# Optimization experiments

Measured on AMD Instinct MI355X. Metric: run time of the kernel, lower is better.

The kernel has to match this reference:

```python
import jax, jax.numpy as jnp
import numpy as np

H = 2880      # hidden_size
NH = 64       # num query heads
NKV = 8       # num kv heads
D = 64        # head_dim
G = NH // NKV # GQA group size
W = 128       # sliding window (keys per query, incl. self)
THETA = 150000.0
N = 1024      # tokens


def setup_inputs() -> dict:
    key = jax.random.key(0)
    k0, k1, k2, k3 = jax.random.split(key, 4)
    hidden_states = jax.random.normal(k0, (N, H), jnp.float32)
    Wqkv = jax.random.normal(k1, (H, (NH + 2 * NKV) * D), jnp.float32) * (H ** -0.5)
    Wo = jax.random.normal(k2, (NH * D, H), jnp.float32) * ((NH * D) ** -0.5)
    sinks = jax.random.normal(k3, (NH,), jnp.float32)
    positions = jnp.arange(N, dtype=jnp.int64)
    return {"hidden_states": hidden_states, "Wqkv": Wqkv, "Wo": Wo,
            "sinks": sinks, "positions": positions}


def _rope(x, pos):
    # NeoX-style rotary over full head_dim. x: [n, h, D], pos: [n]
    half = D // 2
    inv_freq = 1.0 / (THETA ** (jnp.arange(half, dtype=jnp.float32) / half))
    ang = pos[:, None].astype(jnp.float32) * inv_freq          # [n, half]
    cos = jnp.cos(ang)[:, None, :]
    sin = jnp.sin(ang)[:, None, :]
    x1, x2 = x[..., :half], x[..., half:]
    return jnp.concatenate([x1 * cos - x2 * sin, x2 * cos + x1 * sin], axis=-1)


def reference(hidden_states, Wqkv, Wo, sinks, positions):
    n = hidden_states.shape[0]
    qkv = hidden_states @ Wqkv
    q, k, v = jnp.split(qkv, [NH * D, NH * D + NKV * D], axis=-1)
    q = _rope(q.reshape(n, NH, D), positions)   # [n, NH, D]
    k = _rope(k.reshape(n, NKV, D), positions)  # [n, NKV, D]
    v = v.reshape(n, NKV, D)

    # Sliding-window key indices: query i attends keys j in [i-W+1, i]
    idx = positions[:, None] - (W - 1) + jnp.arange(W)[None, :]  # [n, W]
    valid = idx >= 0
    idx = jnp.clip(idx, 0, n - 1)
    k_win = k[idx]  # [n, W, NKV, D]
    v_win = v[idx]  # [n, W, NKV, D]

    qg = q.reshape(n, NKV, G, D)
    scores = jnp.einsum('nkgd,nwkd->nkgw', qg, k_win) * (D ** -0.5)
    scores = jnp.where(valid[:, None, None, :], scores, -jnp.inf)

    # Attention sinks: softmax over [scores, sink_logit]; sink gets no value.
    sink = sinks.reshape(NKV, G)                      # [NKV, G]
    m = jnp.maximum(scores.max(-1), sink[None])       # [n, NKV, G]
    p = jnp.exp(scores - m[..., None])                # [n, NKV, G, W]
    denom = p.sum(-1) + jnp.exp(sink[None] - m)       # [n, NKV, G]
    out = jnp.einsum('nkgw,nwkd->nkgd', p, v_win) / denom[..., None]
    return out.reshape(n, NH * D) @ Wo
```

## Files before the change

kernel.cpp:

```cpp
#include <hip/hip_runtime.h>
#include <hip/hip_bf16.h>

#define HDIM   2880
#define NH     64
#define NKV    8
#define DHEAD  64
#define GQ     (NH / NKV)
#define WIN    128
#define NTOK   1024
#define QKV_N  ((NH + 2 * NKV) * DHEAD)
#define QCOLS  (NH * DHEAD)
#define KOFF   QCOLS
#define VOFF   (QCOLS + NKV * DHEAD)

typedef __attribute__((ext_vector_type(8))) short short8;
typedef __attribute__((ext_vector_type(4))) float floatx4;

__device__ unsigned short g_Xb   [(size_t)NTOK  * HDIM];
__device__ unsigned short g_qkvb [(size_t)NTOK  * QKV_N];
__device__ unsigned short g_attn [(size_t)NTOK  * QCOLS];
__device__ unsigned short g_WqkvT[(size_t)QKV_N * HDIM];
__device__ unsigned short g_WoT  [(size_t)HDIM * QCOLS];

__device__ __forceinline__ unsigned short f2b(float f) {
    __hip_bfloat16 h = __float2bfloat16(f);
    return *reinterpret_cast<unsigned short*>(&h);
}

__device__ __forceinline__ void gload_lds16(const unsigned short* g, unsigned short* l) {
    __builtin_amdgcn_global_load_lds(
        (const __attribute__((address_space(1))) unsigned int*)g,
        (__attribute__((address_space(3))) unsigned int*)l, 16, 0, 0);
}

__global__ __launch_bounds__(256) void transpose_cvt(
        const float* __restrict__ in, unsigned short* __restrict__ out,
        int K, int N) {
    int bk = blockIdx.x, bn = blockIdx.y;
    int t = threadIdx.x;
    __shared__ __align__(16) unsigned short T[64 * 72];
    #pragma unroll
    for (int i = 0; i < 4; ++i) {
        int c = i * 256 + t;
        int r = c >> 4, cc = (c & 15) * 4;
        float4 v = *(const float4*)(in + (size_t)(bk * 64 + r) * N + bn * 64 + cc);
        T[r * 72 + cc + 0] = f2b(v.x);
        T[r * 72 + cc + 1] = f2b(v.y);
        T[r * 72 + cc + 2] = f2b(v.z);
        T[r * 72 + cc + 3] = f2b(v.w);
    }
    __syncthreads();
    #pragma unroll
    for (int i = 0; i < 2; ++i) {
        int c = i * 256 + t;
        int rn = c >> 3, kc = (c & 7) * 8;
        int4 vv;
        unsigned short* tp = (unsigned short*)&vv;
        #pragma unroll
        for (int j = 0; j < 8; ++j) tp[j] = T[(kc + j) * 72 + rn];
        *(int4*)(out + (size_t)(bn * 64 + rn) * K + bk * 64 + kc) = vv;
    }
}

__global__ __launch_bounds__(256) void cvt_bf16(
        const float* __restrict__ in, unsigned short* __restrict__ out, int n4) {
    int id = blockIdx.x * 256 + threadIdx.x;
    if (id >= n4) return;
    float4 v = *(const float4*)(in + (size_t)id * 4);
    ushort4 o;
    o.x = f2b(v.x); o.y = f2b(v.y); o.z = f2b(v.z); o.w = f2b(v.w);
    *(ushort4*)(out + (size_t)id * 4) = o;
}

template<int KLEN, int MODE, int NBN>
__global__ __launch_bounds__(256) void gemm_dir(
        const unsigned short* __restrict__ A, const unsigned short* __restrict__ Bt,
        void* __restrict__ outp) {
    int d0 = blockIdx.x;
    int work = (d0 & 7) * NBN + (d0 >> 3);
    int bm = work & 7, bn = work >> 3;
    int t = threadIdx.x, lane = t & 63, wid = t >> 6;
    int quad = lane >> 4, ml = lane & 15;
    __shared__ __align__(16) unsigned short As[128 * 64];
    __shared__ __align__(16) unsigned short Bs[64 * 64];
    floatx4 acc[2][4];
    #pragma unroll
    for (int i = 0; i < 2; ++i)
        #pragma unroll
        for (int j = 0; j < 4; ++j) acc[i][j] = (floatx4){0.f, 0.f, 0.f, 0.f};

    int srow = lane >> 3;
    int scol = (lane & 7) * 8;
    const unsigned short* Ab = A  + (size_t)(bm * 128) * KLEN;
    const unsigned short* Bb = Bt + (size_t)(bn * 64) * KLEN;

    for (int k0 = 0; k0 < KLEN; k0 += 64) {
        #pragma unroll
        for (int j = 0; j < 4; ++j) {
            int grp = wid * 4 + j;
            int r = grp * 8 + srow;
            gload_lds16(Ab + (size_t)r * KLEN + k0 + scol, &As[grp * 512]);
        }
        #pragma unroll
        for (int j = 0; j < 2; ++j) {
            int grp = wid * 2 + j;
            int r = grp * 8 + srow;
            gload_lds16(Bb + (size_t)r * KLEN + k0 + scol, &Bs[grp * 512]);
        }
        __syncthreads();
        #pragma unroll
        for (int kk = 0; kk < 64; kk += 32) {
            short8 af[2], bf[4];
            #pragma unroll
            for (int mt = 0; mt < 2; ++mt)
                af[mt] = *(const short8*)&As[(wid * 32 + mt * 16 + ml) * 64 + kk + quad * 8];
            #pragma unroll
            for (int nt = 0; nt < 4; ++nt)
                bf[nt] = *(const short8*)&Bs[(nt * 16 + ml) * 64 + kk + quad * 8];
            #pragma unroll
            for (int mt = 0; mt < 2; ++mt)
                #pragma unroll
                for (int nt = 0; nt < 4; ++nt)
                    acc[mt][nt] = __builtin_amdgcn_mfma_f32_16x16x32_bf16(af[mt], bf[nt], acc[mt][nt], 0, 0, 0);
        }
        __syncthreads();
    }

    if constexpr (MODE == 0) {
        unsigned short* qp = (unsigned short*)outp;
        int cb = bn * 64;
        if (bn < NH + NKV) {
            float inv0 = expf(-(float)ml * 0.3724497053f);
            float inv1 = expf(-(float)(16 + ml) * 0.3724497053f);
            #pragma unroll
            for (int mt = 0; mt < 2; ++mt) {
                #pragma unroll
                for (int r = 0; r < 4; ++r) {
                    int n = bm * 128 + wid * 32 + mt * 16 + quad * 4 + r;
                    unsigned short* op = qp + (size_t)n * QKV_N + cb;
                    float s0, c0, s1, c1;
                    sincosf((float)n * inv0, &s0, &c0);
                    sincosf((float)n * inv1, &s1, &c1);
                    float x1a = acc[mt][0][r], x2a = acc[mt][2][r];
                    float x1b = acc[mt][1][r], x2b = acc[mt][3][r];
                    op[ml]           = f2b(x1a * c0 - x2a * s0);
                    op[ml + 32]      = f2b(x2a * c0 + x1a * s0);
                    op[16 + ml]      = f2b(x1b * c1 - x2b * s1);
                    op[16 + ml + 32] = f2b(x2b * c1 + x1b * s1);
                }
            }
        } else {
            #pragma unroll
            for (int mt = 0; mt < 2; ++mt)
                #pragma unroll
                for (int r = 0; r < 4; ++r) {
                    int n = bm * 128 + wid * 32 + mt * 16 + quad * 4 + r;
                    unsigned short* op = qp + (size_t)n * QKV_N + cb;
                    #pragma unroll
                    for (int nt = 0; nt < 4; ++nt)
                        op[nt * 16 + ml] = f2b(acc[mt][nt][r]);
                }
        }
    } else {
        float* op0 = (float*)outp;
        #pragma unroll
        for (int mt = 0; mt < 2; ++mt)
            #pragma unroll
            for (int r = 0; r < 4; ++r) {
                int n = bm * 128 + wid * 32 + mt * 16 + quad * 4 + r;
                float* op = op0 + (size_t)n * HDIM + bn * 64;
                #pragma unroll
                for (int nt = 0; nt < 4; ++nt)
                    op[nt * 16 + ml] = acc[mt][nt][r];
            }
    }
}

#define TQ     16
#define WROWS  160
#define KS_LD  72
#define VT_LD  168
#define PS_LD  168

__global__ __launch_bounds__(256) void attn_mfma(
        const unsigned short* __restrict__ qkvb,
        const float* __restrict__ sinks,
        unsigned short* __restrict__ aout) {
    int d0 = blockIdx.x;
    int work = (d0 & 7) * 64 + (d0 >> 3);
    int t0 = (work & 63) * TQ, kh = work >> 6;
    int t = threadIdx.x, lane = t & 63, wid = t >> 6;
    int quad = lane >> 4, ml = lane & 15;
    int wavebase = wid * 32;

    __shared__ __align__(16) unsigned short Ks[WROWS * KS_LD];
    __shared__ __align__(16) unsigned short Vt[DHEAD * VT_LD];
    __shared__ __align__(16) unsigned short Ps[4 * 16 * PS_LD];
    unsigned short* Psw = &Ps[wid * 16 * PS_LD];

    #pragma unroll
    for (int i = 0; i < 5; ++i) {
        int c = i * 256 + t;
        int w = c >> 3, d8 = (c & 7) * 8;
        int r = t0 - 127 + w;
        r = min(max(r, 0), NTOK - 1);
        *(int4*)&Ks[w * KS_LD + d8] =
            *(const int4*)(qkvb + (size_t)r * QKV_N + KOFF + kh * DHEAD + d8);
        int4 vv = *(const int4*)(qkvb + (size_t)r * QKV_N + VOFF + kh * DHEAD + d8);
        const unsigned short* vp = (const unsigned short*)&vv;
        #pragma unroll
        for (int j = 0; j < 8; ++j) Vt[(d8 + j) * VT_LD + w] = vp[j];
    }
    __syncthreads();

    short8 qf[2][2];
    #pragma unroll
    for (int mt = 0; mt < 2; ++mt) {
        int m = wavebase + mt * 16 + ml;
        int tl = m & 15, g = m >> 4;
        const unsigned short* qp = qkvb + (size_t)(t0 + tl) * QKV_N + (kh * GQ + g) * DHEAD;
        #pragma unroll
        for (int kk = 0; kk < 2; ++kk)
            qf[mt][kk] = *(const short8*)(qp + kk * 32 + quad * 8);
    }

    floatx4 S[2][10];
    #pragma unroll
    for (int mt = 0; mt < 2; ++mt)
        #pragma unroll
        for (int nt = 0; nt < 10; ++nt) S[mt][nt] = (floatx4){0.f, 0.f, 0.f, 0.f};
    #pragma unroll
    for (int kk = 0; kk < 2; ++kk) {
        #pragma unroll
        for (int nt = 0; nt < 10; ++nt) {
            short8 kb = *(const short8*)&Ks[(nt * 16 + ml) * KS_LD + kk * 32 + quad * 8];
            #pragma unroll
            for (int mt = 0; mt < 2; ++mt)
                S[mt][nt] = __builtin_amdgcn_mfma_f32_16x16x32_bf16(qf[mt][kk], kb, S[mt][nt], 0, 0, 0);
        }
    }

    int wmin0 = 127 - t0;
    #pragma unroll
    for (int mt = 0; mt < 2; ++mt) {
        #pragma unroll
        for (int r = 0; r < 4; ++r) {
            int tl = (wavebase + mt * 16 + quad * 4 + r) & 15;
            int wlo = tl > wmin0 ? tl : wmin0;
            int whi = tl + 127;
            #pragma unroll
            for (int nt = 0; nt < 10; ++nt) {
                int w = nt * 16 + ml;
                float s = S[mt][nt][r] * 0.125f;
                S[mt][nt][r] = (w >= wlo && w <= whi) ? s : -INFINITY;
            }
        }
    }

    #pragma unroll
    for (int mt = 0; mt < 2; ++mt) {
        int g = (wavebase + mt * 16) >> 4;
        float sk = sinks[kh * GQ + g];
        #pragma unroll
        for (int r = 0; r < 4; ++r) {
            float rm = -INFINITY;
            #pragma unroll
            for (int nt = 0; nt < 10; ++nt) rm = fmaxf(rm, S[mt][nt][r]);
            #pragma unroll
            for (int off = 1; off < 16; off <<= 1) rm = fmaxf(rm, __shfl_xor(rm, off));
            rm = fmaxf(rm, sk);
            float sum = 0.f;
            #pragma unroll
            for (int nt = 0; nt < 10; ++nt) {
                float p = __expf(S[mt][nt][r] - rm);
                S[mt][nt][r] = p;
                sum += p;
            }
            #pragma unroll
            for (int off = 1; off < 16; off <<= 1) sum += __shfl_xor(sum, off);
            float inv = 1.f / (sum + __expf(sk - rm));
            #pragma unroll
            for (int nt = 0; nt < 10; ++nt) S[mt][nt][r] *= inv;
        }
    }

    #pragma unroll
    for (int mt = 0; mt < 2; ++mt) {
        #pragma unroll
        for (int r = 0; r < 4; ++r) {
            int lr = quad * 4 + r;
            #pragma unroll
            for (int nt = 0; nt < 10; ++nt)
                Psw[lr * PS_LD + nt * 16 + ml] = f2b(S[mt][nt][r]);
        }
        floatx4 O[4];
        #pragma unroll
        for (int j = 0; j < 4; ++j) O[j] = (floatx4){0.f, 0.f, 0.f, 0.f};
        #pragma unroll
        for (int ks = 0; ks < 5; ++ks) {
            short8 pf = *(const short8*)&Psw[ml * PS_LD + ks * 32 + quad * 8];
            #pragma unroll
            for (int nt = 0; nt < 4; ++nt) {
                short8 vf = *(const short8*)&Vt[(nt * 16 + ml) * VT_LD + ks * 32 + quad * 8];
                O[nt] = __builtin_amdgcn_mfma_f32_16x16x32_bf16(pf, vf, O[nt], 0, 0, 0);
            }
        }
        #pragma unroll
        for (int r = 0; r < 4; ++r) {
            int mm = wavebase + mt * 16 + quad * 4 + r;
            int tl = mm & 15, g = mm >> 4;
            unsigned short* op = aout + (size_t)(t0 + tl) * QCOLS + (kh * GQ + g) * DHEAD;
            #pragma unroll
            for (int nt = 0; nt < 4; ++nt)
                op[nt * 16 + ml] = f2b(O[nt][r]);
        }
    }
}

extern "C" void kernel_launch(void* const* d_in, const int* in_sizes, int n_in,
                              void* d_out, int out_size, void* d_ws, size_t ws_size,
                              hipStream_t stream) {
    const float* X     = (const float*)d_in[0];
    const float* Wqkv  = (const float*)d_in[1];
    const float* Wo    = (const float*)d_in[2];
    const float* sinks = (const float*)d_in[3];
    float* out = (float*)d_out;

    unsigned short *Xb, *qkvb, *attn, *WqkvT, *WoT;
    hipGetSymbolAddress((void**)&Xb,    HIP_SYMBOL(g_Xb));
    hipGetSymbolAddress((void**)&qkvb,  HIP_SYMBOL(g_qkvb));
    hipGetSymbolAddress((void**)&attn,  HIP_SYMBOL(g_attn));
    hipGetSymbolAddress((void**)&WqkvT, HIP_SYMBOL(g_WqkvT));
    hipGetSymbolAddress((void**)&WoT,   HIP_SYMBOL(g_WoT));

    cvt_bf16<<<(NTOK * HDIM / 4 + 255) / 256, 256, 0, stream>>>(X, Xb, NTOK * HDIM / 4);
    transpose_cvt<<<dim3(HDIM / 64, QKV_N / 64), 256, 0, stream>>>(Wqkv, WqkvT, HDIM, QKV_N);
    transpose_cvt<<<dim3(QCOLS / 64, HDIM / 64), 256, 0, stream>>>(Wo, WoT, QCOLS, HDIM);

    gemm_dir<HDIM, 0, QKV_N / 64><<<8 * (QKV_N / 64), 256, 0, stream>>>(Xb, WqkvT, qkvb);

    attn_mfma<<<512, 256, 0, stream>>>(qkvb, sinks, attn);

    gemm_dir<QCOLS, 1, HDIM / 64><<<8 * (HDIM / 64), 256, 0, stream>>>(attn, WoT, out);
}
```

Measured before the change: 315.9 us.

## Double-buffer GEMM LDS tiles and XOR-swizzle to avoid bank conflicts

The GEMM kernel now keeps two LDS buffers for the A and B tiles. The next k-tile is loaded directly from global memory into LDS while the MFMA work runs on the current tile. The LDS layout is also XOR-swizzled per row, and the read addresses are adjusted to match, to reduce bank conflicts on the short8 fragment loads. This doubles LDS use per block, which may lower occupancy, and relies on correct synchronisation around buffer reuse.

```diff
diff --git a/kernel.cpp b/kernel.cpp
--- a/kernel.cpp
+++ b/kernel.cpp
@@ -81,8 +81,8 @@
     int bm = work & 7, bn = work >> 3;
     int t = threadIdx.x, lane = t & 63, wid = t >> 6;
     int quad = lane >> 4, ml = lane & 15;
-    __shared__ __align__(16) unsigned short As[128 * 64];
-    __shared__ __align__(16) unsigned short Bs[64 * 64];
+    __shared__ __align__(16) unsigned short As[2][128 * 64];
+    __shared__ __align__(16) unsigned short Bs[2][64 * 64];
     floatx4 acc[2][4];
     #pragma unroll
     for (int i = 0; i < 2; ++i)
@@ -90,33 +90,55 @@
         for (int j = 0; j < 4; ++j) acc[i][j] = (floatx4){0.f, 0.f, 0.f, 0.f};
 
     int srow = lane >> 3;
-    int scol = (lane & 7) * 8;
+    int scol = ((lane & 7) ^ srow) * 8;
     const unsigned short* Ab = A  + (size_t)(bm * 128) * KLEN;
     const unsigned short* Bb = Bt + (size_t)(bn * 64) * KLEN;
 
-    for (int k0 = 0; k0 < KLEN; k0 += 64) {
-        #pragma unroll
-        for (int j = 0; j < 4; ++j) {
-            int grp = wid * 4 + j;
-            int r = grp * 8 + srow;
-            gload_lds16(Ab + (size_t)r * KLEN + k0 + scol, &As[grp * 512]);
-        }
-        #pragma unroll
-        for (int j = 0; j < 2; ++j) {
-            int grp = wid * 2 + j;
-            int r = grp * 8 + srow;
-            gload_lds16(Bb + (size_t)r * KLEN + k0 + scol, &Bs[grp * 512]);
-        }
-        __syncthreads();
+    constexpr int NT = KLEN / 64;
+
+    #pragma unroll
+    for (int j = 0; j < 4; ++j) {
+        int grp = wid * 4 + j;
+        int r = grp * 8 + srow;
+        gload_lds16(Ab + (size_t)r * KLEN + scol, &As[0][grp * 512]);
+    }
+    #pragma unroll
+    for (int j = 0; j < 2; ++j) {
+        int grp = wid * 2 + j;
+        int r = grp * 8 + srow;
+        gload_lds16(Bb + (size_t)r * KLEN + scol, &Bs[0][grp * 512]);
+    }
+    __syncthreads();
+
+    for (int ti = 0; ti < NT; ++ti) {
+        int cur = ti & 1;
+        if (ti + 1 < NT) {
+            int k0 = (ti + 1) * 64;
+            int nxt = cur ^ 1;
+            #pragma unroll
+            for (int j = 0; j < 4; ++j) {
+                int grp = wid * 4 + j;
+                int r = grp * 8 + srow;
+                gload_lds16(Ab + (size_t)r * KLEN + k0 + scol, &As[nxt][grp * 512]);
+            }
+            #pragma unroll
+            for (int j = 0; j < 2; ++j) {
+                int grp = wid * 2 + j;
+                int r = grp * 8 + srow;
+                gload_lds16(Bb + (size_t)r * KLEN + k0 + scol, &Bs[nxt][grp * 512]);
+            }
+        }
         #pragma unroll
         for (int kk = 0; kk < 64; kk += 32) {
+            const int ub = kk >> 3;
+            int usw = ((ub + quad) ^ (ml & 7)) * 8;
             short8 af[2], bf[4];
             #pragma unroll
             for (int mt = 0; mt < 2; ++mt)
-                af[mt] = *(const short8*)&As[(wid * 32 + mt * 16 + ml) * 64 + kk + quad * 8];
+                af[mt] = *(const short8*)&As[cur][(wid * 32 + mt * 16 + ml) * 64 + usw];
             #pragma unroll
             for (int nt = 0; nt < 4; ++nt)
-                bf[nt] = *(const short8*)&Bs[(nt * 16 + ml) * 64 + kk + quad * 8];
+                bf[nt] = *(const short8*)&Bs[cur][(nt * 16 + ml) * 64 + usw];
             #pragma unroll
             for (int mt = 0; mt < 2; ++mt)
                 #pragma unroll
```

Measured after the change: 312.0 us. No clear change (-1.2%).

## Triple-buffer GEMM LDS tiles with async prefetch and XOR-swizzled layout

Applied to the files above, without the earlier changes.

The GEMM main loop now keeps three LDS buffers and issues global-to-LDS loads two tiles ahead, waiting with a partial vmcnt and a single barrier per iteration instead of two syncthreads. The LDS layout is XOR-swizzled by row to reduce bank conflicts on the MFMA fragment reads. This is meant to hide global load latency behind MFMA work. In exchange it triples LDS use, which may lower occupancy, and correctness depends on the hand-counted vmcnt value matching the number of outstanding loads.

```diff
diff --git a/kernel.cpp b/kernel.cpp
--- a/kernel.cpp
+++ b/kernel.cpp
@@ -81,8 +81,8 @@
     int bm = work & 7, bn = work >> 3;
     int t = threadIdx.x, lane = t & 63, wid = t >> 6;
     int quad = lane >> 4, ml = lane & 15;
-    __shared__ __align__(16) unsigned short As[128 * 64];
-    __shared__ __align__(16) unsigned short Bs[64 * 64];
+    __shared__ __align__(16) unsigned short As[3][128 * 64];
+    __shared__ __align__(16) unsigned short Bs[3][64 * 64];
     floatx4 acc[2][4];
     #pragma unroll
     for (int i = 0; i < 2; ++i)
@@ -90,40 +90,54 @@
         for (int j = 0; j < 4; ++j) acc[i][j] = (floatx4){0.f, 0.f, 0.f, 0.f};
 
     int srow = lane >> 3;
-    int scol = (lane & 7) * 8;
+    int scol = ((lane & 7) ^ srow) * 8;
     const unsigned short* Ab = A  + (size_t)(bm * 128) * KLEN;
     const unsigned short* Bb = Bt + (size_t)(bn * 64) * KLEN;
 
-    for (int k0 = 0; k0 < KLEN; k0 += 64) {
+    constexpr int NT = KLEN / 64;
+
+    auto STAGE = [&](int ti, int buf) {
+        int k0 = ti * 64;
         #pragma unroll
         for (int j = 0; j < 4; ++j) {
             int grp = wid * 4 + j;
             int r = grp * 8 + srow;
-            gload_lds16(Ab + (size_t)r * KLEN + k0 + scol, &As[grp * 512]);
+            gload_lds16(Ab + (size_t)r * KLEN + k0 + scol, &As[buf][grp * 512]);
         }
         #pragma unroll
         for (int j = 0; j < 2; ++j) {
             int grp = wid * 2 + j;
             int r = grp * 8 + srow;
-            gload_lds16(Bb + (size_t)r * KLEN + k0 + scol, &Bs[grp * 512]);
-        }
-        __syncthreads();
+            gload_lds16(Bb + (size_t)r * KLEN + k0 + scol, &Bs[buf][grp * 512]);
+        }
+    };
+
+    STAGE(0, 0);
+    STAGE(1, 1);
+
+    for (int ti = 0; ti < NT; ++ti) {
+        if (ti + 1 < NT) asm volatile("s_waitcnt vmcnt(6)" ::: "memory");
+        else             asm volatile("s_waitcnt vmcnt(0)" ::: "memory");
+        __builtin_amdgcn_s_barrier();
+        if (ti + 2 < NT) STAGE(ti + 2, (ti + 2) % 3);
+        int cur = ti % 3;
         #pragma unroll
         for (int kk = 0; kk < 64; kk += 32) {
+            const int ub = kk >> 3;
+            int usw = ((ub + quad) ^ (ml & 7)) * 8;
             short8 af[2], bf[4];
             #pragma unroll
             for (int mt = 0; mt < 2; ++mt)
-                af[mt] = *(const short8*)&As[(wid * 32 + mt * 16 + ml) * 64 + kk + quad * 8];
+                af[mt] = *(const short8*)&As[cur][(wid * 32 + mt * 16 + ml) * 64 + usw];
             #pragma unroll
             for (int nt = 0; nt < 4; ++nt)
-                bf[nt] = *(const short8*)&Bs[(nt * 16 + ml) * 64 + kk + quad * 8];
+                bf[nt] = *(const short8*)&Bs[cur][(nt * 16 + ml) * 64 + usw];
             #pragma unroll
             for (int mt = 0; mt < 2; ++mt)
                 #pragma unroll
                 for (int nt = 0; nt < 4; ++nt)
                     acc[mt][nt] = __builtin_amdgcn_mfma_f32_16x16x32_bf16(af[mt], bf[nt], acc[mt][nt], 0, 0, 0);
         }
-        __syncthreads();
     }
 
     if constexpr (MODE == 0) {
```

New measurement: 303.6 us. -3.9%, faster.
